# Kernel optimization log

Hardware: AMD Instinct MI355X
Metric: run time of the kernel (lower is better)

Reference implementation:

```python
import jax, jax.numpy as jnp
import numpy as np

GAMMA = 0.01   # module default gamma
STEP = 10      # forward subsamples time axis with x[::10]
BIG = 1e10     # finite stand-in for +inf boundary (exp(-BIG/gamma) underflows to 0 exactly)


def _softdtw(D, gamma):
    """Batched soft-DTW DP over cost matrices D: (B, N, M) -> (B,).
    Anti-diagonal wavefront: lax.scan over the 2*max(N,M)-1 diagonals,
    each diagonal updated fully vectorized (mirrors compute_softdtw_cuda).
    """
    B, N, M = D.shape
    inv_g = 1.0 / gamma
    # padded R, boundaries at BIG (acts as +inf), R[:,0,0] = 0
    R0 = jnp.full((B, N + 2, M + 2), BIG, dtype=D.dtype).at[:, 0, 0].set(0.0)
    ii = jnp.arange(1, N + 1)  # padded row indices on a diagonal

    def step(R, p):
        jj = p + 2 - ii                      # i + j = p + 2 in padded coords
        valid = (jj >= 1) & (jj <= M)
        jc = jnp.clip(jj, 1, M)
        r0 = -R[:, ii - 1, jc - 1] * inv_g   # diag neighbor
        r1 = -R[:, ii - 1, jc] * inv_g       # up neighbor
        r2 = -R[:, ii, jc - 1] * inv_g       # left neighbor
        rmax = jnp.maximum(jnp.maximum(r0, r1), r2)
        rsum = jnp.exp(r0 - rmax) + jnp.exp(r1 - rmax) + jnp.exp(r2 - rmax)
        softmin = -gamma * (jnp.log(rsum) + rmax)
        new = D[:, ii - 1, jc - 1] + softmin
        R = R.at[:, ii, jc].set(jnp.where(valid[None, :], new, R[:, ii, jc]))
        return R, None

    R, _ = jax.lax.scan(step, R0, jnp.arange(N + M - 1))
    return R[:, N, M]


def _loss(x, y):
    # x, y: (nt, nr, nc). Subsample time by STEP; treat each (r, c) trace as a
    # batch-1, dim-1 sequence; sum soft-DTW values over all nr*nc traces.
    xs = x[::STEP]                      # (L, nr, nc)
    ys = y[::STEP]
    L = xs.shape[0]
    X = xs.reshape(L, -1).T             # (B, L), B = nr*nc
    Y = ys.reshape(L, -1).T
    D = (X[:, :, None] - Y[:, None, :]) ** 2  # squared-Euclidean cost, d=1
    return jnp.sum(_softdtw(D, GAMMA)).reshape(1)


def setup_inputs() -> dict:
    key = jax.random.key(0)
    k1, k2 = jax.random.split(key)
    x = jax.random.normal(k1, (2048, 128, 2), dtype=jnp.float32)
    y = jax.random.normal(k2, (2048, 128, 2), dtype=jnp.float32)
    return {"x": x, "y": y}


def reference(x, y):
    return _loss(x, y)
```

## Files before the change

### kernel.cpp

```cpp
#include <hip/hip_runtime.h>

#define STEP 10
#define NCH  256
#define CSCL (-144.2695041f)
#define GLN2 (-0.00693147181f)
#define BIGP (-1.442695041e12f)
#define YOFF 64
#define YLDS 384
#define BNDSZ 472
#define NW   4

__device__ __forceinline__ float fexp2(float x){ float r; asm("v_exp_f32 %0, %1" : "=v"(r) : "v"(x)); return r; }
__device__ __forceinline__ float flog2(float x){ float r; asm("v_log_f32 %0, %1" : "=v"(r) : "v"(x)); return r; }

__device__ __forceinline__ float dpp_shr1(float src){
    int s = __builtin_bit_cast(int, src);
    int r = __builtin_amdgcn_update_dpp(0, s, 0x138 , 0xF, 0xF, true);
    return __builtin_bit_cast(float, r);
}

__device__ __forceinline__ float dpcell(float up2, float up, float left,
                                        float xv, float yv) {
    float m  = fmaxf(fmaxf(up2, up), left);
    float lo = fminf(fminf(up2, up), left);
    float md = __builtin_amdgcn_fmed3f(up2, up, left);
    float e  = fexp2(lo - m) + fexp2(md - m) + 1.0f;
    float ls = flog2(e) + m;
    float d  = xv - yv;
    return fmaf(d * CSCL, d, ls);
}

__global__ __launch_bounds__(256)
void softdtw_wave(const float* __restrict__ x, const float* __restrict__ y,
                  float* __restrict__ ws, int N) {
    const int b = blockIdx.x;
    const int t = threadIdx.x;
    const int l = t & 63;
    const int w = t >> 6;

    __shared__ __align__(16) float Ys[YLDS];
    __shared__ float bnd[NW - 1][BNDSZ];
    __shared__ int prog[NW - 1];

    for (int j = t; j < YLDS; j += 256) Ys[j] = 0.f;
    float* bf = &bnd[0][0];
    for (int j = t; j < (NW - 1) * BNDSZ; j += 256) bf[j] = BIGP;
    if (t < NW - 1) prog[t] = 0;
    __syncthreads();
    for (int j = t; j < N; j += 256) Ys[YOFF + j] = y[j * STEP * NCH + b];
    __syncthreads();

    const int i = 64 * w + l + 1;
    const float xv = (i <= N) ? x[(i - 1) * STEP * NCH + b] : 0.f;

    float sp = BIGP, bp = BIGP;
    float bq = (t == 0) ? 0.0f : BIGP;

    const int smax = 2 * N;
    const int NG   = (N + 63 + 7) >> 3;
    const int sb0  = 64 * w + 2;
    const bool prod = (w < NW - 1);
    const bool cons = (w > 0);
    const int progFinal = 64 * (w - 1) + 2 + NG * 8 - 1;

    const float* yb = Ys + (YOFF - l);

    #define STEPJ(YV, HJ, CJ, J) do {                              \
        CJ = dpcell(bq, bp, sp, xv, (YV));                         \
        float sh = dpp_shr1(CJ);                                   \
        bq = bp;                                                   \
        bp = (l == 0) ? (HJ) : sh;                                 \
        sp = CJ;                                                   \
        if (sb + (J) == smax) { if (i == N) ws[b] = CJ * GLN2; }   \
    } while (0)

    for (int m = 0; m < NG; ++m) {
        const int sb = sb0 + 8 * m;
        float y0 = yb[0], y1 = yb[1], y2 = yb[2], y3 = yb[3];
        float y4 = yb[4], y5 = yb[5], y6 = yb[6], y7 = yb[7];
        yb += 8;

        float h0, h1, h2, h3, h4, h5, h6, h7;
        if (cons) {
            const int need = min(sb + 7, progFinal);
            while (__hip_atomic_load(&prog[w - 1], __ATOMIC_ACQUIRE,
                                     __HIP_MEMORY_SCOPE_WORKGROUP) < need)
                __builtin_amdgcn_s_sleep(1);
            const float* bb = bnd[w - 1];
            if (m == 0 && l == 0) bp = bb[sb - 1];
            h0 = bb[sb + 0]; h1 = bb[sb + 1]; h2 = bb[sb + 2]; h3 = bb[sb + 3];
            h4 = bb[sb + 4]; h5 = bb[sb + 5]; h6 = bb[sb + 6]; h7 = bb[sb + 7];
        } else {
            h0 = h1 = h2 = h3 = h4 = h5 = h6 = h7 = BIGP;
        }

        float c0, c1, c2, c3, c4, c5, c6, c7;
        STEPJ(y0, h0, c0, 0); STEPJ(y1, h1, c1, 1);
        STEPJ(y2, h2, c2, 2); STEPJ(y3, h3, c3, 3);
        STEPJ(y4, h4, c4, 4); STEPJ(y5, h5, c5, 5);
        STEPJ(y6, h6, c6, 6); STEPJ(y7, h7, c7, 7);

        if (prod && l == 63) {
            float* bw = &bnd[w][sb];
            bw[0] = c0; bw[1] = c1; bw[2] = c2; bw[3] = c3;
            bw[4] = c4; bw[5] = c5; bw[6] = c6; bw[7] = c7;
            __hip_atomic_store(&prog[w], sb + 7, __ATOMIC_RELEASE,
                               __HIP_MEMORY_SCOPE_WORKGROUP);
        }
    }
    #undef STEPJ
}

__global__ __launch_bounds__(256)
void reduce256(const float* __restrict__ ws, float* __restrict__ out) {
    const int tid = threadIdx.x;
    float v = ws[tid];
    #pragma unroll
    for (int off = 32; off > 0; off >>= 1)
        v += __shfl_down(v, off, 64);
    __shared__ float partial[4];
    if ((tid & 63) == 0) partial[tid >> 6] = v;
    __syncthreads();
    if (tid == 0) out[0] = (partial[0] + partial[1]) + (partial[2] + partial[3]);
}

extern "C" void kernel_launch(void* const* d_in, const int* in_sizes, int n_in,
                              void* d_out, int out_size, void* d_ws, size_t ws_size,
                              hipStream_t stream) {
    const float* x = (const float*)d_in[0];
    const float* y = (const float*)d_in[1];
    float* out = (float*)d_out;
    float* ws  = (float*)d_ws;

    const int T = in_sizes[0] / NCH;
    const int L = (T + STEP - 1) / STEP;

    softdtw_wave<<<dim3(NCH), dim3(256), 0, stream>>>(x, y, ws, L);
    reduce256<<<dim3(1), dim3(256), 0, stream>>>(ws, out);
}
```

Measured before the change: 43.03 us.

## Process two soft-DTW traces per workgroup to interleave independent dependency chains

Each workgroup now computes two batch traces (A and B) at once, interleaving their DP cell updates so the two independent serial chains can hide each other's exp/log/DPP latency. The grid is halved to 128 blocks, and shared-memory boundaries and progress flags are duplicated. The cost is fewer workgroups, which on a GPU with more CUs than blocks leaves more CUs idle, plus more registers per lane and doubled LDS traffic.

```diff
diff --git a/kernel.cpp b/kernel.cpp
--- a/kernel.cpp
+++ b/kernel.cpp
@@ -33,28 +33,33 @@
 __global__ __launch_bounds__(256)
 void softdtw_wave(const float* __restrict__ x, const float* __restrict__ y,
                   float* __restrict__ ws, int N) {
-    const int b = blockIdx.x;
+    const int b0 = blockIdx.x * 2;
+    const int b1 = b0 + 1;
     const int t = threadIdx.x;
     const int l = t & 63;
     const int w = t >> 6;
 
-    __shared__ __align__(16) float Ys[YLDS];
-    __shared__ float bnd[NW - 1][BNDSZ];
-    __shared__ int prog[NW - 1];
+    __shared__ __align__(16) float YsA[YLDS], YsB[YLDS];
+    __shared__ float bndA[NW - 1][BNDSZ], bndB[NW - 1][BNDSZ];
+    __shared__ int progA[NW - 1], progB[NW - 1];
 
-    for (int j = t; j < YLDS; j += 256) Ys[j] = 0.f;
-    float* bf = &bnd[0][0];
-    for (int j = t; j < (NW - 1) * BNDSZ; j += 256) bf[j] = BIGP;
-    if (t < NW - 1) prog[t] = 0;
+    for (int j = t; j < YLDS; j += 256) { YsA[j] = 0.f; YsB[j] = 0.f; }
+    float* bfA = &bndA[0][0]; float* bfB = &bndB[0][0];
+    for (int j = t; j < (NW - 1) * BNDSZ; j += 256) { bfA[j] = BIGP; bfB[j] = BIGP; }
+    if (t < NW - 1) { progA[t] = 0; progB[t] = 0; }
     __syncthreads();
-    for (int j = t; j < N; j += 256) Ys[YOFF + j] = y[j * STEP * NCH + b];
+    for (int j = t; j < N; j += 256) {
+        YsA[YOFF + j] = y[j * STEP * NCH + b0];
+        YsB[YOFF + j] = y[j * STEP * NCH + b1];
+    }
     __syncthreads();
 
     const int i = 64 * w + l + 1;
-    const float xv = (i <= N) ? x[(i - 1) * STEP * NCH + b] : 0.f;
+    const float xvA = (i <= N) ? x[(i - 1) * STEP * NCH + b0] : 0.f;
+    const float xvB = (i <= N) ? x[(i - 1) * STEP * NCH + b1] : 0.f;
 
-    float sp = BIGP, bp = BIGP;
-    float bq = (t == 0) ? 0.0f : BIGP;
+    float spA = BIGP, bpA = BIGP, bqA = (t == 0) ? 0.0f : BIGP;
+    float spB = BIGP, bpB = BIGP, bqB = (t == 0) ? 0.0f : BIGP;
 
     const int smax = 2 * N;
     const int NG   = (N + 63 + 7) >> 3;
@@ -63,52 +68,77 @@
     const bool cons = (w > 0);
     const int progFinal = 64 * (w - 1) + 2 + NG * 8 - 1;
 
-    const float* yb = Ys + (YOFF - l);
+    const float* ybA = YsA + (YOFF - l);
+    const float* ybB = YsB + (YOFF - l);
 
-    #define STEPJ(YV, HJ, CJ, J) do {                              \
-        CJ = dpcell(bq, bp, sp, xv, (YV));                         \
-        float sh = dpp_shr1(CJ);                                   \
-        bq = bp;                                                   \
-        bp = (l == 0) ? (HJ) : sh;                                 \
-        sp = CJ;                                                   \
-        if (sb + (J) == smax) { if (i == N) ws[b] = CJ * GLN2; }   \
+    #define STEPJ2(YA, HA, CA, YB, HB, CB, J) do {                  \
+        CA = dpcell(bqA, bpA, spA, xvA, (YA));                      \
+        CB = dpcell(bqB, bpB, spB, xvB, (YB));                      \
+        float shA = dpp_shr1(CA);                                   \
+        float shB = dpp_shr1(CB);                                   \
+        bqA = bpA; bqB = bpB;                                       \
+        bpA = (l == 0) ? (HA) : shA;                                \
+        bpB = (l == 0) ? (HB) : shB;                                \
+        spA = CA; spB = CB;                                         \
+        if (sb + (J) == smax && i == N) {                           \
+            ws[b0] = CA * GLN2; ws[b1] = CB * GLN2;                 \
+        }                                                           \
     } while (0)
 
     for (int m = 0; m < NG; ++m) {
         const int sb = sb0 + 8 * m;
-        float y0 = yb[0], y1 = yb[1], y2 = yb[2], y3 = yb[3];
-        float y4 = yb[4], y5 = yb[5], y6 = yb[6], y7 = yb[7];
-        yb += 8;
+        float yA0 = ybA[0], yA1 = ybA[1], yA2 = ybA[2], yA3 = ybA[3];
+        float yA4 = ybA[4], yA5 = ybA[5], yA6 = ybA[6], yA7 = ybA[7];
+        float yB0 = ybB[0], yB1 = ybB[1], yB2 = ybB[2], yB3 = ybB[3];
+        float yB4 = ybB[4], yB5 = ybB[5], yB6 = ybB[6], yB7 = ybB[7];
+        ybA += 8; ybB += 8;
 
-        float h0, h1, h2, h3, h4, h5, h6, h7;
+        float hA0,hA1,hA2,hA3,hA4,hA5,hA6,hA7;
+        float hB0,hB1,hB2,hB3,hB4,hB5,hB6,hB7;
         if (cons) {
             const int need = min(sb + 7, progFinal);
-            while (__hip_atomic_load(&prog[w - 1], __ATOMIC_ACQUIRE,
+            while (__hip_atomic_load(&progA[w - 1], __ATOMIC_ACQUIRE,
+                                     __HIP_MEMORY_SCOPE_WORKGROUP) < need ||
+                   __hip_atomic_load(&progB[w - 1], __ATOMIC_ACQUIRE,
                                      __HIP_MEMORY_SCOPE_WORKGROUP) < need)
                 __builtin_amdgcn_s_sleep(1);
-            const float* bb = bnd[w - 1];
-            if (m == 0 && l == 0) bp = bb[sb - 1];
-            h0 = bb[sb + 0]; h1 = bb[sb + 1]; h2 = bb[sb + 2]; h3 = bb[sb + 3];
-            h4 = bb[sb + 4]; h5 = bb[sb + 5]; h6 = bb[sb + 6]; h7 = bb[sb + 7];
+            const float* bbA = bndA[w - 1];
+            const float* bbB = bndB[w - 1];
+            if (m == 0 && l == 0) { bpA = bbA[sb - 1]; bpB = bbB[sb - 1]; }
+            hA0 = bbA[sb+0]; hA1 = bbA[sb+1]; hA2 = bbA[sb+2]; hA3 = bbA[sb+3];
+            hA4 = bbA[sb+4]; hA5 = bbA[sb+5]; hA6 = bbA[sb+6]; hA7 = bbA[sb+7];
+            hB0 = bbB[sb+0]; hB1 = bbB[sb+1]; hB2 = bbB[sb+2]; hB3 = bbB[sb+3];
+            hB4 = bbB[sb+4]; hB5 = bbB[sb+5]; hB6 = bbB[sb+6]; hB7 = bbB[sb+7];
         } else {
-            h0 = h1 = h2 = h3 = h4 = h5 = h6 = h7 = BIGP;
+            hA0=hA1=hA2=hA3=hA4=hA5=hA6=hA7 = BIGP;
+            hB0=hB1=hB2=hB3=hB4=hB5=hB6=hB7 = BIGP;
         }
 
-        float c0, c1, c2, c3, c4, c5, c6, c7;
-        STEPJ(y0, h0, c0, 0); STEPJ(y1, h1, c1, 1);
-        STEPJ(y2, h2, c2, 2); STEPJ(y3, h3, c3, 3);
-        STEPJ(y4, h4, c4, 4); STEPJ(y5, h5, c5, 5);
-        STEPJ(y6, h6, c6, 6); STEPJ(y7, h7, c7, 7);
+        float cA0,cA1,cA2,cA3,cA4,cA5,cA6,cA7;
+        float cB0,cB1,cB2,cB3,cB4,cB5,cB6,cB7;
+        STEPJ2(yA0,hA0,cA0, yB0,hB0,cB0, 0);
+        STEPJ2(yA1,hA1,cA1, yB1,hB1,cB1, 1);
+        STEPJ2(yA2,hA2,cA2, yB2,hB2,cB2, 2);
+        STEPJ2(yA3,hA3,cA3, yB3,hB3,cB3, 3);
+        STEPJ2(yA4,hA4,cA4, yB4,hB4,cB4, 4);
+        STEPJ2(yA5,hA5,cA5, yB5,hB5,cB5, 5);
+        STEPJ2(yA6,hA6,cA6, yB6,hB6,cB6, 6);
+        STEPJ2(yA7,hA7,cA7, yB7,hB7,cB7, 7);
 
         if (prod && l == 63) {
-            float* bw = &bnd[w][sb];
-            bw[0] = c0; bw[1] = c1; bw[2] = c2; bw[3] = c3;
-            bw[4] = c4; bw[5] = c5; bw[6] = c6; bw[7] = c7;
-            __hip_atomic_store(&prog[w], sb + 7, __ATOMIC_RELEASE,
+            float* bwA = &bndA[w][sb];
+            bwA[0]=cA0; bwA[1]=cA1; bwA[2]=cA2; bwA[3]=cA3;
+            bwA[4]=cA4; bwA[5]=cA5; bwA[6]=cA6; bwA[7]=cA7;
+            float* bwB = &bndB[w][sb];
+            bwB[0]=cB0; bwB[1]=cB1; bwB[2]=cB2; bwB[3]=cB3;
+            bwB[4]=cB4; bwB[5]=cB5; bwB[6]=cB6; bwB[7]=cB7;
+            __hip_atomic_store(&progA[w], sb + 7, __ATOMIC_RELEASE,
+                               __HIP_MEMORY_SCOPE_WORKGROUP);
+            __hip_atomic_store(&progB[w], sb + 7, __ATOMIC_RELEASE,
                                __HIP_MEMORY_SCOPE_WORKGROUP);
         }
     }
-    #undef STEPJ
+    #undef STEPJ2
 }
 
 __global__ __launch_bounds__(256)
@@ -135,6 +165,6 @@
     const int T = in_sizes[0] / NCH;
     const int L = (T + STEP - 1) / STEP;
 
-    softdtw_wave<<<dim3(NCH), dim3(256), 0, stream>>>(x, y, ws, L);
+    softdtw_wave<<<dim3(NCH / 2), dim3(256), 0, stream>>>(x, y, ws, L);
     reduce256<<<dim3(1), dim3(256), 0, stream>>>(ws, out);
 }
```

New measurement: 65.08 us. 1.51x slower.

## Precompute scaled costs ahead of each chunk and trim per-wave diagonal count

Applied to the files above, without the earlier changes.

The squared-distance cost for the next 8 columns is computed before the current chunk finishes, and the boundary polling and loads are moved ahead too, so the serial DP recurrence carries only a max/exp/log/add chain. The number of diagonal groups per wave is now derived from that wave's own row range, which skips groups past the last valid diagonal. Launch bounds are set to one block per CU. This adds register pressure and makes the consumer wait on the producer one group earlier.

```diff
diff --git a/kernel.cpp b/kernel.cpp
--- a/kernel.cpp
+++ b/kernel.cpp
@@ -19,18 +19,16 @@
     return __builtin_bit_cast(float, r);
 }
 
-__device__ __forceinline__ float dpcell(float up2, float up, float left,
-                                        float xv, float yv) {
+__device__ __forceinline__ float dpcell(float up2, float up, float left, float qq) {
     float m  = fmaxf(fmaxf(up2, up), left);
     float lo = fminf(fminf(up2, up), left);
     float md = __builtin_amdgcn_fmed3f(up2, up, left);
     float e  = fexp2(lo - m) + fexp2(md - m) + 1.0f;
-    float ls = flog2(e) + m;
-    float d  = xv - yv;
-    return fmaf(d * CSCL, d, ls);
+    float mq = m + qq;
+    return flog2(e) + mq;
 }
 
-__global__ __launch_bounds__(256)
+__global__ __launch_bounds__(256, 1)
 void softdtw_wave(const float* __restrict__ x, const float* __restrict__ y,
                   float* __restrict__ ws, int N) {
     const int b = blockIdx.x;
@@ -57,58 +55,88 @@
     float bq = (t == 0) ? 0.0f : BIGP;
 
     const int smax = 2 * N;
-    const int NG   = (N + 63 + 7) >> 3;
     const int sb0  = 64 * w + 2;
+    const int myrows = (64 * (w + 1) < N) ? 64 * (w + 1) : N;
+    const int NG     = (myrows + N - sb0 + 1 + 7) >> 3;
     const bool prod = (w < NW - 1);
     const bool cons = (w > 0);
-    const int progFinal = 64 * (w - 1) + 2 + NG * 8 - 1;
+    const int prows = (64 * w < N) ? 64 * w : N;
+    const int pNG   = (prows + N - (sb0 - 64) + 1 + 7) >> 3;
+    const int progFinal = (sb0 - 64) + 8 * pNG - 1;
 
     const float* yb = Ys + (YOFF - l);
+    const float* bb = cons ? bnd[w - 1] : bnd[0];
 
-    #define STEPJ(YV, HJ, CJ, J) do {                              \
-        CJ = dpcell(bq, bp, sp, xv, (YV));                         \
+    #define POLL(NEED) do {                                               \
+        const int need_ = min((NEED), progFinal);                         \
+        while (__hip_atomic_load(&prog[w - 1], __ATOMIC_ACQUIRE,          \
+                                 __HIP_MEMORY_SCOPE_WORKGROUP) < need_)   \
+            __builtin_amdgcn_s_sleep(1);                                  \
+    } while (0)
+
+    float q0,q1,q2,q3,q4,q5,q6,q7;
+    float h0,h1,h2,h3,h4,h5,h6,h7;
+    {
+        float a0=yb[0],a1=yb[1],a2=yb[2],a3=yb[3];
+        float a4=yb[4],a5=yb[5],a6=yb[6],a7=yb[7];
+        if (cons) {
+            POLL(sb0 + 7);
+            if (l == 0) bp = bb[sb0 - 1];
+            h0=bb[sb0+0]; h1=bb[sb0+1]; h2=bb[sb0+2]; h3=bb[sb0+3];
+            h4=bb[sb0+4]; h5=bb[sb0+5]; h6=bb[sb0+6]; h7=bb[sb0+7];
+        } else {
+            h0=h1=h2=h3=h4=h5=h6=h7 = BIGP;
+        }
+        float d;
+        d=xv-a0; q0=d*CSCL*d;  d=xv-a1; q1=d*CSCL*d;
+        d=xv-a2; q2=d*CSCL*d;  d=xv-a3; q3=d*CSCL*d;
+        d=xv-a4; q4=d*CSCL*d;  d=xv-a5; q5=d*CSCL*d;
+        d=xv-a6; q6=d*CSCL*d;  d=xv-a7; q7=d*CSCL*d;
+    }
+
+    #define STEPJ(QQ, HJ, CJ, J) do {                              \
+        CJ = dpcell(bq, bp, sp, (QQ));                             \
         float sh = dpp_shr1(CJ);                                   \
         bq = bp;                                                   \
         bp = (l == 0) ? (HJ) : sh;                                 \
         sp = CJ;                                                   \
-        if (sb + (J) == smax) { if (i == N) ws[b] = CJ * GLN2; }   \
+        if (sb + (J) == smax && i == N) ws[b] = CJ * GLN2;         \
     } while (0)
 
     for (int m = 0; m < NG; ++m) {
         const int sb = sb0 + 8 * m;
-        float y0 = yb[0], y1 = yb[1], y2 = yb[2], y3 = yb[3];
-        float y4 = yb[4], y5 = yb[5], y6 = yb[6], y7 = yb[7];
-        yb += 8;
-
-        float h0, h1, h2, h3, h4, h5, h6, h7;
-        if (cons) {
-            const int need = min(sb + 7, progFinal);
-            while (__hip_atomic_load(&prog[w - 1], __ATOMIC_ACQUIRE,
-                                     __HIP_MEMORY_SCOPE_WORKGROUP) < need)
-                __builtin_amdgcn_s_sleep(1);
-            const float* bb = bnd[w - 1];
-            if (m == 0 && l == 0) bp = bb[sb - 1];
-            h0 = bb[sb + 0]; h1 = bb[sb + 1]; h2 = bb[sb + 2]; h3 = bb[sb + 3];
-            h4 = bb[sb + 4]; h5 = bb[sb + 5]; h6 = bb[sb + 6]; h7 = bb[sb + 7];
-        } else {
-            h0 = h1 = h2 = h3 = h4 = h5 = h6 = h7 = BIGP;
-        }
-
-        float c0, c1, c2, c3, c4, c5, c6, c7;
-        STEPJ(y0, h0, c0, 0); STEPJ(y1, h1, c1, 1);
-        STEPJ(y2, h2, c2, 2); STEPJ(y3, h3, c3, 3);
-        STEPJ(y4, h4, c4, 4); STEPJ(y5, h5, c5, 5);
-        STEPJ(y6, h6, c6, 6); STEPJ(y7, h7, c7, 7);
+        float c0,c1,c2,c3,c4,c5,c6,c7;
+        STEPJ(q0, h0, c0, 0); STEPJ(q1, h1, c1, 1);
+        STEPJ(q2, h2, c2, 2); STEPJ(q3, h3, c3, 3);
+        STEPJ(q4, h4, c4, 4); STEPJ(q5, h5, c5, 5);
+        STEPJ(q6, h6, c6, 6); STEPJ(q7, h7, c7, 7);
 
         if (prod && l == 63) {
             float* bw = &bnd[w][sb];
-            bw[0] = c0; bw[1] = c1; bw[2] = c2; bw[3] = c3;
-            bw[4] = c4; bw[5] = c5; bw[6] = c6; bw[7] = c7;
+            bw[0]=c0; bw[1]=c1; bw[2]=c2; bw[3]=c3;
+            bw[4]=c4; bw[5]=c5; bw[6]=c6; bw[7]=c7;
             __hip_atomic_store(&prog[w], sb + 7, __ATOMIC_RELEASE,
                                __HIP_MEMORY_SCOPE_WORKGROUP);
         }
+
+        if (m + 1 < NG) {
+            const float* yn = yb + 8 * (m + 1);
+            float a0=yn[0],a1=yn[1],a2=yn[2],a3=yn[3];
+            float a4=yn[4],a5=yn[5],a6=yn[6],a7=yn[7];
+            if (cons) {
+                POLL(sb + 15);
+                h0=bb[sb+8];  h1=bb[sb+9];  h2=bb[sb+10]; h3=bb[sb+11];
+                h4=bb[sb+12]; h5=bb[sb+13]; h6=bb[sb+14]; h7=bb[sb+15];
+            }
+            float d;
+            d=xv-a0; q0=d*CSCL*d;  d=xv-a1; q1=d*CSCL*d;
+            d=xv-a2; q2=d*CSCL*d;  d=xv-a3; q3=d*CSCL*d;
+            d=xv-a4; q4=d*CSCL*d;  d=xv-a5; q5=d*CSCL*d;
+            d=xv-a6; q6=d*CSCL*d;  d=xv-a7; q7=d*CSCL*d;
+        }
     }
     #undef STEPJ
+    #undef POLL
 }
 
 __global__ __launch_bounds__(256)
```

New measurement: 38.17 us. 1.13x faster.
